# Kernel tuning notes

Measured on AMD Instinct MI355X. Metric: run time of the kernel, lower is better.

Reference implementation:

```python
import jax, jax.numpy as jnp
import numpy as np

NUM_GRAPHS = 64
NUM_LAYERS = 3
HEADS = 4
HID = 64
DMODEL = HEADS * HID  # 256
NUM_EDGE_TYPES = 8
NUM_CLASSES = 2
N_NODES = 30000
N_EDGES = 240000


def setup_inputs() -> dict:
    key = jax.random.key(0)
    ks = jax.random.split(key, 16)
    s = 0.05
    x = jax.random.normal(ks[0], (N_NODES, DMODEL), jnp.float32)
    edge_index = jax.random.randint(ks[1], (2, N_EDGES), 0, N_NODES)
    batch = jnp.sort(jax.random.randint(ks[2], (N_NODES,), 0, NUM_GRAPHS))
    edge_type_ids = jax.random.randint(ks[3], (N_EDGES,), 0, NUM_EDGE_TYPES)
    # stacked per-layer conv params (all layers are DMODEL -> HEADS*HID = DMODEL)
    Wq = jax.random.normal(ks[4], (NUM_LAYERS, DMODEL, DMODEL), jnp.float32) * s
    bq = jax.random.normal(ks[5], (NUM_LAYERS, DMODEL), jnp.float32) * s
    Wk = jax.random.normal(ks[6], (NUM_LAYERS, DMODEL, DMODEL), jnp.float32) * s
    bk = jax.random.normal(ks[7], (NUM_LAYERS, DMODEL), jnp.float32) * s
    Wv = jax.random.normal(ks[8], (NUM_LAYERS, DMODEL, DMODEL), jnp.float32) * s
    bv = jax.random.normal(ks[9], (NUM_LAYERS, DMODEL), jnp.float32) * s
    Eemb = jax.random.normal(ks[10], (NUM_LAYERS, NUM_EDGE_TYPES, DMODEL), jnp.float32) * s
    # 1-layer GRU (PyTorch layout: [3*hid, in], gate order r, z, n)
    W_ih = jax.random.normal(ks[11], (3 * HID, DMODEL), jnp.float32) * s
    b_ih = jax.random.normal(ks[12], (3 * HID,), jnp.float32) * s
    W_hh = jax.random.normal(ks[13], (3 * HID, HID), jnp.float32) * s
    b_hh = jax.random.normal(ks[14], (3 * HID,), jnp.float32) * s
    W_fc = jax.random.normal(ks[15], (NUM_CLASSES, HID), jnp.float32) * s
    b_fc = jnp.zeros((NUM_CLASSES,), jnp.float32)
    return dict(x=x, edge_index=edge_index, batch=batch, edge_type_ids=edge_type_ids,
                Wq=Wq, bq=bq, Wk=Wk, bk=bk, Wv=Wv, bv=bv, Eemb=Eemb,
                W_ih=W_ih, b_ih=b_ih, W_hh=W_hh, b_hh=b_hh, W_fc=W_fc, b_fc=b_fc)


def reference(x, edge_index, batch, edge_type_ids, Wq, bq, Wk, bk, Wv, bv, Eemb,
              W_ih, b_ih, W_hh, b_hh, W_fc, b_fc):
    N = x.shape[0]
    src, dst = edge_index[0], edge_index[1]  # messages flow src -> dst
    scale = 1.0 / jnp.sqrt(jnp.float32(HID))
    for l in range(NUM_LAYERS):
        q = (x @ Wq[l] + bq[l]).reshape(N, HEADS, HID)
        k_all = x @ Wk[l] + bk[l]  # [N, DMODEL]
        v_all = x @ Wv[l] + bv[l]
        ete = Eemb[l][edge_type_ids]  # edge-type conditioning, [E, DMODEL]
        k = (k_all[src] + ete).reshape(-1, HEADS, HID)
        v = (v_all[src] + ete).reshape(-1, HEADS, HID)
        scores = jnp.einsum('ehd,ehd->eh', q[dst], k) * scale  # [E, H]
        # per-destination-node segment softmax (stable)
        m = jax.ops.segment_max(scores, dst, num_segments=N)
        ex = jnp.exp(scores - m[dst])
        den = jax.ops.segment_sum(ex, dst, num_segments=N)
        alpha = ex / (den[dst] + 1e-16)
        agg = jax.ops.segment_sum(alpha[..., None] * v, dst, num_segments=N)
        x = jax.nn.elu(agg.reshape(N, DMODEL))
    # global mean pool over graphs
    cnt = jax.ops.segment_sum(jnp.ones((N,), x.dtype), batch, num_segments=NUM_GRAPHS)
    g = jax.ops.segment_sum(x, batch, num_segments=NUM_GRAPHS) / jnp.maximum(cnt, 1.0)[:, None]
    # single GRU step from h0 = 0 (seq_len == 1)
    h0 = jnp.zeros((NUM_GRAPHS, HID), x.dtype)
    gi = g @ W_ih.T + b_ih
    gh = h0 @ W_hh.T + b_hh
    ir, iz, inn = jnp.split(gi, 3, axis=-1)
    hr, hz, hn = jnp.split(gh, 3, axis=-1)
    r = jax.nn.sigmoid(ir + hr)
    z = jax.nn.sigmoid(iz + hz)
    n = jnp.tanh(inn + r * hn)
    h = (1.0 - z) * n + z * h0
    return h @ W_fc.T + b_fc  # [NUM_GRAPHS, NUM_CLASSES]
```

## Files before the change

### kernel.cpp

```cpp
#include <hip/hip_runtime.h>
#include <math.h>

#define N_NODES 30000
#define N_EDGES 240000
#define DMODEL 256
#define NETYPES 8
#define NGRAPHS 64
#define NLAYERS 3

typedef __attribute__((ext_vector_type(8))) short short8;
typedef __attribute__((ext_vector_type(4))) float f32x4;

__device__ __forceinline__ unsigned short f2bf(float f) {
  union { float f; unsigned u; } v; v.f = f;
  unsigned r = v.u + 0x7FFF + ((v.u >> 16) & 1);
  return (unsigned short)(r >> 16);
}
__device__ __forceinline__ float bf2f(unsigned short h) {
  union { unsigned u; float f; } v; v.u = ((unsigned)h) << 16;
  return v.f;
}

__device__ __forceinline__ void async_g2l(const unsigned short* g, unsigned short* l) {
  __builtin_amdgcn_global_load_lds(
      (const __attribute__((address_space(1))) void*)g,
      (__attribute__((address_space(3))) void*)l, 16, 0, 0);
}

__global__ void k_count_deg(const int* __restrict__ dst, int* __restrict__ deg) {
  int e = blockIdx.x * blockDim.x + threadIdx.x;
  if (e < N_EDGES) atomicAdd(&deg[dst[e]], 1);
}

__global__ __launch_bounds__(1024) void k_scan(const int* __restrict__ deg,
                                               int* __restrict__ rowstart,
                                               int* __restrict__ cursor) {
  const int C = 30;
  int tid = threadIdx.x;
  int base = tid * C;
  int vals[C];
  int sum = 0;
#pragma unroll
  for (int j = 0; j < C; ++j) {
    int idx = base + j;
    int v = (idx < N_NODES) ? deg[idx] : 0;
    vals[j] = sum;
    sum += v;
  }
  int lane = tid & 63, wv = tid >> 6;
  int s = sum;
#pragma unroll
  for (int off = 1; off < 64; off <<= 1) {
    int t2 = __shfl_up(s, off);
    if (lane >= off) s += t2;
  }
  __shared__ int wsum[16];
  if (lane == 63) wsum[wv] = s;
  __syncthreads();
  if (tid == 0) {
    int a = 0;
#pragma unroll
    for (int i = 0; i < 16; ++i) { int t2 = wsum[i]; wsum[i] = a; a += t2; }
    rowstart[N_NODES] = a;
  }
  __syncthreads();
  int texcl = wsum[wv] + (s - sum);
#pragma unroll
  for (int j = 0; j < C; ++j) {
    int idx = base + j;
    if (idx < N_NODES) {
      int p = texcl + vals[j];
      rowstart[idx] = p;
      cursor[idx]   = p;
    }
  }
}

__global__ void k_scatter(const int* __restrict__ src, const int* __restrict__ dst,
                          const int* __restrict__ etype, int* __restrict__ cursor,
                          int* __restrict__ packed) {
  int e = blockIdx.x * blockDim.x + threadIdx.x;
  if (e < N_EDGES) {
    int p = atomicAdd(&cursor[dst[e]], 1);
    packed[p] = src[e] * NETYPES + etype[e];
  }
}

__global__ __launch_bounds__(256) void k_cvt_w(
    const float* __restrict__ Wq, const float* __restrict__ Wk, const float* __restrict__ Wv,
    unsigned short* __restrict__ wthi) {
  __shared__ float tile[32][33];
  int k0 = blockIdx.x * 32;
  int n0g = blockIdx.y * 32;
  int l = blockIdx.z;
  int which = n0g >> 8;
  int col0 = n0g & 255;
  const float* W = (which == 0) ? Wq : ((which == 1) ? Wk : Wv);
  int c = threadIdx.x & 31, r = threadIdx.x >> 5;
#pragma unroll
  for (int rr = 0; rr < 4; ++rr) {
    int kk = r + rr * 8;
    tile[kk][c] = W[(size_t)l * 65536 + (size_t)(k0 + kk) * 256 + col0 + c];
  }
  __syncthreads();
  int kk = threadIdx.x & 31, nn0 = threadIdx.x >> 5;
#pragma unroll
  for (int rr = 0; rr < 4; ++rr) {
    int nn = nn0 + rr * 8;
    wthi[((size_t)l * 768 + n0g + nn) * 256 + k0 + kk] = f2bf(tile[kk][nn]);
  }
}

__global__ void k_cvt_b(const float* __restrict__ bq, const float* __restrict__ bk,
                        const float* __restrict__ bv, float* __restrict__ bcat) {
  int idx = blockIdx.x * 256 + threadIdx.x;
  if (idx >= NLAYERS * 768) return;
  int n = idx % 768, l = idx / 768;
  int which = n >> 8, col = n & 255;
  const float* b = (which == 0) ? bq : ((which == 1) ? bk : bv);
  bcat[idx] = b[l * 256 + col];
}

__global__ void k_cvt_x(const float* __restrict__ x, unsigned short* __restrict__ xhi,
                        unsigned short* __restrict__ xlo) {
  int i = blockIdx.x * 256 + threadIdx.x;
  if (i < N_NODES * 256) {
    float v = x[i];
    unsigned short h = f2bf(v);
    xhi[i] = h;
    xlo[i] = f2bf(v - bf2f(h));
  }
}

__global__ __launch_bounds__(256) void k_gemm_mfma(
    const unsigned short* __restrict__ Ahi, const unsigned short* __restrict__ Alo,
    const unsigned short* __restrict__ Bhi,
    const float* __restrict__ bcat, float* __restrict__ qbuf,
    unsigned short* __restrict__ kv) {
  __shared__ unsigned short smem[2 * 12288];

  int tid = threadIdx.x;
  int lane = tid & 63, wave = tid >> 6;
  int bx = blockIdx.x;
  int xcd = bx & 7, slot = bx >> 3;
  int rt = xcd + (slot / 6) * 8;
  if (rt >= 235) return;
  int row0 = rt * 128;
  int n0 = (slot % 6) * 128;
  int wm = (wave >> 1) * 64, wn = (wave & 1) * 64;
  int quad = lane >> 4, l16 = lane & 15;
  int chunk = lane & 3;
  int srow = wave * 32 + (lane >> 2);

  f32x4 acc[4][4];
#pragma unroll
  for (int i = 0; i < 4; ++i)
#pragma unroll
    for (int j = 0; j < 4; ++j) acc[i][j] = (f32x4)(0.f);

  auto STAGE = [&](int k0, int b) {
    unsigned short* s = smem + b * 12288;
#pragma unroll
    for (int j = 0; j < 2; ++j) {
      int r = srow + j * 16;
      int ldsoff = wave * 1024 + j * 512;
      int garA = row0 + r; if (garA >= N_NODES) garA = N_NODES - 1;
      size_t aoff = (size_t)garA * 256 + k0 + chunk * 8;
      async_g2l(Ahi + aoff, s + ldsoff);
      async_g2l(Alo + aoff, s + 4096 + ldsoff);
      size_t boff = (size_t)(n0 + r) * 256 + k0 + chunk * 8;
      async_g2l(Bhi + boff, s + 8192 + ldsoff);
    }
  };

  STAGE(0, 0);
#pragma unroll
  for (int k = 0; k < 8; ++k) {
    int cur = k & 1;
    if (k < 7) {
      STAGE((k + 1) * 32, cur ^ 1);
      asm volatile("s_waitcnt vmcnt(6)" ::: "memory");
    } else {
      asm volatile("s_waitcnt vmcnt(0)" ::: "memory");
    }
    __builtin_amdgcn_s_barrier();

    const unsigned short* sAhi = smem + cur * 12288;
    const unsigned short* sAlo = sAhi + 4096;
    const unsigned short* sBhi = sAhi + 8192;
    short8 ah[4], al[4], bh[4];
#pragma unroll
    for (int i = 0; i < 4; ++i) {
      int off = (wm + i * 16 + l16) * 32 + quad * 8;
      ah[i] = *(const short8*)(sAhi + off);
      al[i] = *(const short8*)(sAlo + off);
    }
#pragma unroll
    for (int j = 0; j < 4; ++j) {
      int off = (wn + j * 16 + l16) * 32 + quad * 8;
      bh[j] = *(const short8*)(sBhi + off);
    }
#pragma unroll
    for (int i = 0; i < 4; ++i)
#pragma unroll
      for (int j = 0; j < 4; ++j) {
        acc[i][j] = __builtin_amdgcn_mfma_f32_16x16x32_bf16(ah[i], bh[j], acc[i][j], 0, 0, 0);
        acc[i][j] = __builtin_amdgcn_mfma_f32_16x16x32_bf16(al[i], bh[j], acc[i][j], 0, 0, 0);
      }
    __builtin_amdgcn_s_barrier();
  }

  float bj[4];
#pragma unroll
  for (int j = 0; j < 4; ++j) bj[j] = bcat[n0 + wn + j * 16 + l16];
  bool isq = (n0 < 256);
#pragma unroll
  for (int i = 0; i < 4; ++i) {
    int rowb = row0 + wm + i * 16 + quad * 4;
#pragma unroll
    for (int r = 0; r < 4; ++r) {
      int grow = rowb + r;
      if (grow < N_NODES) {
        if (isq) {
          float* cp = qbuf + (size_t)grow * 256 + n0 + wn + l16;
#pragma unroll
          for (int j = 0; j < 4; ++j) cp[j * 16] = acc[i][j][r] + bj[j];
        } else {
          unsigned short* cp = kv + (size_t)grow * 512 + (n0 - 256) + wn + l16;
#pragma unroll
          for (int j = 0; j < 4; ++j) cp[j * 16] = f2bf(acc[i][j][r] + bj[j]);
        }
      }
    }
  }
}

__global__ __launch_bounds__(256) void k_attn(
    const float* __restrict__ qbuf, const unsigned short* __restrict__ kv,
    const int* __restrict__ rowstart, const int* __restrict__ packed,
    const float* __restrict__ Eemb_l,
    unsigned short* __restrict__ xhi, unsigned short* __restrict__ xlo) {
  __shared__ float ete_s[NETYPES * 256];
  int t = threadIdx.x;
#pragma unroll
  for (int i = 0; i < NETYPES; ++i) ete_s[i * 256 + t] = Eemb_l[i * 256 + t];
  __syncthreads();
  int lane = t & 63;
  int n = blockIdx.x * 4 + (t >> 6);
  float4 q4 = ((const float4*)(qbuf + (size_t)n * 256))[lane];
  int rs = rowstart[n], re = rowstart[n + 1];
  float l1 = 0.f, ax1 = 0.f, ay1 = 0.f, az1 = 0.f, aw1 = 0.f;
  float l2 = 0.f, ax2 = 0.f, ay2 = 0.f, az2 = 0.f, aw2 = 0.f;
  int i = rs;
  for (; i + 2 <= re; i += 2) {
    int pkA = packed[i], pkB = packed[i + 1];
    const unsigned short* baseA = kv + (size_t)(pkA >> 3) * 512;
    const unsigned short* baseB = kv + (size_t)(pkB >> 3) * 512;
    ushort4 kA = ((const ushort4*)baseA)[lane];
    ushort4 vA = ((const ushort4*)(baseA + 256))[lane];
    ushort4 kB = ((const ushort4*)baseB)[lane];
    ushort4 vB = ((const ushort4*)(baseB + 256))[lane];
    float4 eA = ((const float4*)(ete_s + (pkA & 7) * 256))[lane];
    float4 eB = ((const float4*)(ete_s + (pkB & 7) * 256))[lane];
    float pA = (bf2f(kA.x) + eA.x) * q4.x + (bf2f(kA.y) + eA.y) * q4.y +
               (bf2f(kA.z) + eA.z) * q4.z + (bf2f(kA.w) + eA.w) * q4.w;
    float pB = (bf2f(kB.x) + eB.x) * q4.x + (bf2f(kB.y) + eB.y) * q4.y +
               (bf2f(kB.z) + eB.z) * q4.z + (bf2f(kB.w) + eB.w) * q4.w;
    pA += __shfl_xor(pA, 1); pB += __shfl_xor(pB, 1);
    pA += __shfl_xor(pA, 2); pB += __shfl_xor(pB, 2);
    pA += __shfl_xor(pA, 4); pB += __shfl_xor(pB, 4);
    pA += __shfl_xor(pA, 8); pB += __shfl_xor(pB, 8);
    float e1 = __expf(pA * 0.125f);
    float e2 = __expf(pB * 0.125f);
    l1 += e1; l2 += e2;
    ax1 = fmaf(e1, bf2f(vA.x) + eA.x, ax1);
    ay1 = fmaf(e1, bf2f(vA.y) + eA.y, ay1);
    az1 = fmaf(e1, bf2f(vA.z) + eA.z, az1);
    aw1 = fmaf(e1, bf2f(vA.w) + eA.w, aw1);
    ax2 = fmaf(e2, bf2f(vB.x) + eB.x, ax2);
    ay2 = fmaf(e2, bf2f(vB.y) + eB.y, ay2);
    az2 = fmaf(e2, bf2f(vB.z) + eB.z, az2);
    aw2 = fmaf(e2, bf2f(vB.w) + eB.w, aw2);
  }
  if (i < re) {
    int pk = packed[i];
    const unsigned short* base = kv + (size_t)(pk >> 3) * 512;
    ushort4 kh = ((const ushort4*)base)[lane];
    ushort4 vh = ((const ushort4*)(base + 256))[lane];
    float4 e4 = ((const float4*)(ete_s + (pk & 7) * 256))[lane];
    float p = (bf2f(kh.x) + e4.x) * q4.x + (bf2f(kh.y) + e4.y) * q4.y +
              (bf2f(kh.z) + e4.z) * q4.z + (bf2f(kh.w) + e4.w) * q4.w;
    p += __shfl_xor(p, 1);
    p += __shfl_xor(p, 2);
    p += __shfl_xor(p, 4);
    p += __shfl_xor(p, 8);
    float e1 = __expf(p * 0.125f);
    l1 += e1;
    ax1 = fmaf(e1, bf2f(vh.x) + e4.x, ax1);
    ay1 = fmaf(e1, bf2f(vh.y) + e4.y, ay1);
    az1 = fmaf(e1, bf2f(vh.z) + e4.z, az1);
    aw1 = fmaf(e1, bf2f(vh.w) + e4.w, aw1);
  }
  float l = l1 + l2;
  float inv = 1.f / (l + 1e-16f);
  float4 o;
  o.x = (ax1 + ax2) * inv; o.y = (ay1 + ay2) * inv;
  o.z = (az1 + az2) * inv; o.w = (aw1 + aw2) * inv;
  o.x = o.x > 0.f ? o.x : expm1f(o.x);
  o.y = o.y > 0.f ? o.y : expm1f(o.y);
  o.z = o.z > 0.f ? o.z : expm1f(o.z);
  o.w = o.w > 0.f ? o.w : expm1f(o.w);
  unsigned short h0 = f2bf(o.x), h1 = f2bf(o.y), h2 = f2bf(o.z), h3 = f2bf(o.w);
  ushort4 hv, lv;
  hv.x = h0; hv.y = h1; hv.z = h2; hv.w = h3;
  lv.x = f2bf(o.x - bf2f(h0)); lv.y = f2bf(o.y - bf2f(h1));
  lv.z = f2bf(o.z - bf2f(h2)); lv.w = f2bf(o.w - bf2f(h3));
  size_t base_o = (size_t)n * 256 + lane * 4;
  *(ushort4*)(xhi + base_o) = hv;
  *(ushort4*)(xlo + base_o) = lv;
}

__global__ __launch_bounds__(256) void k_pool_partial(
    const unsigned short* __restrict__ xhi, const unsigned short* __restrict__ xlo,
    const int* __restrict__ batch, float* __restrict__ gacc) {
  int t = threadIdx.x;
  int base = blockIdx.x * 128;
  int end = base + 128; if (end > N_NODES) end = N_NODES;
  __shared__ int bsh[128];
  if (t < 128 && base + t < N_NODES) bsh[t] = batch[base + t];
  __syncthreads();
  float acc = 0.f;
  int cur = bsh[0];
  for (int n = base; n < end; ++n) {
    int g = bsh[n - base];
    if (g != cur) {
      atomicAdd(&gacc[cur * 256 + t], acc);
      acc = 0.f; cur = g;
    }
    size_t idx = (size_t)n * 256 + t;
    acc += bf2f(xhi[idx]) + bf2f(xlo[idx]);
  }
  atomicAdd(&gacc[cur * 256 + t], acc);
}

__device__ inline int lower_bound_dev(const int* a, int n, int val) {
  int lo = 0, hi = n;
  while (lo < hi) {
    int mid = (lo + hi) >> 1;
    if (a[mid] < val) lo = mid + 1; else hi = mid;
  }
  return lo;
}

__global__ __launch_bounds__(256) void k_gru_fc(
    const float* __restrict__ gacc, const int* __restrict__ batch,
    const float* __restrict__ W_ih, const float* __restrict__ b_ih,
    const float* __restrict__ b_hh, const float* __restrict__ W_fc,
    const float* __restrict__ b_fc, float* __restrict__ out) {
  __shared__ float gv[256];
  __shared__ float gates[192];
  __shared__ float h[64];
  int gr = blockIdx.x, t = threadIdx.x;
  int s0 = lower_bound_dev(batch, N_NODES, gr);
  int e0 = lower_bound_dev(batch, N_NODES, gr + 1);
  float c = (e0 > s0) ? (float)(e0 - s0) : 1.f;
  gv[t] = gacc[gr * 256 + t] / c;
  __syncthreads();
  if (t < 192) {
    const float* wr = W_ih + t * 256;
    float s = b_ih[t];
    for (int k = 0; k < 256; ++k) s = fmaf(gv[k], wr[k], s);
    gates[t] = s;
  }
  __syncthreads();
  if (t < 64) {
    float r  = 1.f / (1.f + expf(-(gates[t] + b_hh[t])));
    float z  = 1.f / (1.f + expf(-(gates[64 + t] + b_hh[64 + t])));
    float nn = tanhf(gates[128 + t] + r * b_hh[128 + t]);
    h[t] = (1.f - z) * nn;
  }
  __syncthreads();
  if (t < 2) {
    const float* wr = W_fc + t * 64;
    float s = b_fc[t];
    for (int k = 0; k < 64; ++k) s = fmaf(h[k], wr[k], s);
    out[gr * 2 + t] = s;
  }
}

extern "C" void kernel_launch(void* const* d_in, const int* in_sizes, int n_in,
                              void* d_out, int out_size, void* d_ws, size_t ws_size,
                              hipStream_t stream) {
  const float* x     = (const float*)d_in[0];
  const int* edge_index = (const int*)d_in[1];
  const int* batch   = (const int*)d_in[2];
  const int* etype   = (const int*)d_in[3];
  const float* Wq    = (const float*)d_in[4];
  const float* bq    = (const float*)d_in[5];
  const float* Wk    = (const float*)d_in[6];
  const float* bk    = (const float*)d_in[7];
  const float* Wv    = (const float*)d_in[8];
  const float* bv    = (const float*)d_in[9];
  const float* Eemb  = (const float*)d_in[10];
  const float* W_ih  = (const float*)d_in[11];
  const float* b_ih  = (const float*)d_in[12];
  const float* b_hh  = (const float*)d_in[14];
  const float* W_fc  = (const float*)d_in[15];
  const float* b_fc  = (const float*)d_in[16];
  float* out = (float*)d_out;

  const int* src = edge_index;
  const int* dst = edge_index + N_EDGES;

  float* qbuf  = (float*)d_ws;
  float* gacc  = qbuf + (size_t)N_NODES * 256;
  float* bcat  = gacc + NGRAPHS * 256;
  unsigned short* kv   = (unsigned short*)(bcat + NLAYERS * 768);
  unsigned short* xhi  = kv + (size_t)N_NODES * 512;
  unsigned short* xlo  = xhi + (size_t)N_NODES * 256;
  unsigned short* wthi = xlo + (size_t)N_NODES * 256;
  int* deg      = (int*)(wthi + (size_t)NLAYERS * 768 * 256);
  int* rowstart = deg + N_NODES;
  int* cursor   = rowstart + N_NODES + 1;
  int* packed   = cursor + N_NODES;

  hipMemsetAsync(deg, 0, N_NODES * sizeof(int), stream);
  hipMemsetAsync(gacc, 0, NGRAPHS * 256 * sizeof(float), stream);
  k_count_deg<<<(N_EDGES + 255) / 256, 256, 0, stream>>>(dst, deg);
  k_scan<<<1, 1024, 0, stream>>>(deg, rowstart, cursor);
  k_scatter<<<(N_EDGES + 255) / 256, 256, 0, stream>>>(src, dst, etype, cursor, packed);

  k_cvt_w<<<dim3(8, 24, 3), 256, 0, stream>>>(Wq, Wk, Wv, wthi);
  k_cvt_b<<<(NLAYERS * 768 + 255) / 256, 256, 0, stream>>>(bq, bk, bv, bcat);
  k_cvt_x<<<(N_NODES * 256 + 255) / 256, 256, 0, stream>>>(x, xhi, xlo);

  for (int l = 0; l < NLAYERS; ++l) {
    k_gemm_mfma<<<1440, 256, 0, stream>>>(
        xhi, xlo, wthi + (size_t)l * 768 * 256,
        bcat + l * 768, qbuf, kv);
    k_attn<<<N_NODES / 4, 256, 0, stream>>>(qbuf, kv, rowstart, packed,
                                            Eemb + (size_t)l * NETYPES * 256, xhi, xlo);
  }
  k_pool_partial<<<(N_NODES + 127) / 128, 256, 0, stream>>>(xhi, xlo, batch, gacc);
  k_gru_fc<<<NGRAPHS, 256, 0, stream>>>(gacc, batch, W_ih, b_ih, b_hh, W_fc, b_fc, out);
}
```

Before: 461.8 us.

## Software-pipeline edge gathers in attention kernel with wave-wide index prefetch

The attention kernel now loads up to 64 edge indices per destination node in one coalesced wave load and broadcasts them with shuffles. It then double-buffers K/V/edge-embedding gathers in groups of four edges, issuing the next group's loads before computing the current one. This is meant to hide gather latency by keeping more memory requests in flight. In exchange it uses more registers, which may lower occupancy, and nodes with more than 64 edges fall back to a serial tail loop.

```diff
diff --git a/kernel.cpp b/kernel.cpp
--- a/kernel.cpp
+++ b/kernel.cpp
@@ -235,6 +235,36 @@
   }
 }
 
+#define LOAD1(pk, K, V, E)                                       \
+  { const unsigned short* b_ = kv + (size_t)((pk) >> 3) * 512;   \
+    K = ((const ushort4*)b_)[lane];                              \
+    V = ((const ushort4*)(b_ + 256))[lane];                      \
+    E = ((const float4*)(ete_s + ((pk) & 7) * 256))[lane]; }
+
+#define EDGE1(K, V, E)                                                 \
+  { float p_ = (bf2f(K.x) + E.x) * q4.x + (bf2f(K.y) + E.y) * q4.y +   \
+               (bf2f(K.z) + E.z) * q4.z + (bf2f(K.w) + E.w) * q4.w;    \
+    p_ += __shfl_xor(p_, 1); p_ += __shfl_xor(p_, 2);                  \
+    p_ += __shfl_xor(p_, 4); p_ += __shfl_xor(p_, 8);                  \
+    float e_ = __expf(p_ * 0.125f);                                    \
+    lsum += e_;                                                        \
+    ax = fmaf(e_, bf2f(V.x) + E.x, ax);                                \
+    ay = fmaf(e_, bf2f(V.y) + E.y, ay);                                \
+    az = fmaf(e_, bf2f(V.z) + E.z, az);                                \
+    aw = fmaf(e_, bf2f(V.w) + E.w, aw); }
+
+#define LOAD4(s, c)                                                    \
+  { int p0_ = __shfl(mypk, (c));     int p1_ = __shfl(mypk, (c) + 1);  \
+    int p2_ = __shfl(mypk, (c) + 2); int p3_ = __shfl(mypk, (c) + 3);  \
+    LOAD1(p0_, k##s##0, v##s##0, e##s##0)                              \
+    LOAD1(p1_, k##s##1, v##s##1, e##s##1)                              \
+    LOAD1(p2_, k##s##2, v##s##2, e##s##2)                              \
+    LOAD1(p3_, k##s##3, v##s##3, e##s##3) }
+
+#define COMP4(s)                                                        \
+    EDGE1(k##s##0, v##s##0, e##s##0) EDGE1(k##s##1, v##s##1, e##s##1)   \
+    EDGE1(k##s##2, v##s##2, e##s##2) EDGE1(k##s##3, v##s##3, e##s##3)
+
 __global__ __launch_bounds__(256) void k_attn(
     const float* __restrict__ qbuf, const unsigned short* __restrict__ kv,
     const int* __restrict__ rowstart, const int* __restrict__ packed,
@@ -249,63 +279,48 @@
   int n = blockIdx.x * 4 + (t >> 6);
   float4 q4 = ((const float4*)(qbuf + (size_t)n * 256))[lane];
   int rs = rowstart[n], re = rowstart[n + 1];
-  float l1 = 0.f, ax1 = 0.f, ay1 = 0.f, az1 = 0.f, aw1 = 0.f;
-  float l2 = 0.f, ax2 = 0.f, ay2 = 0.f, az2 = 0.f, aw2 = 0.f;
-  int i = rs;
-  for (; i + 2 <= re; i += 2) {
-    int pkA = packed[i], pkB = packed[i + 1];
-    const unsigned short* baseA = kv + (size_t)(pkA >> 3) * 512;
-    const unsigned short* baseB = kv + (size_t)(pkB >> 3) * 512;
-    ushort4 kA = ((const ushort4*)baseA)[lane];
-    ushort4 vA = ((const ushort4*)(baseA + 256))[lane];
-    ushort4 kB = ((const ushort4*)baseB)[lane];
-    ushort4 vB = ((const ushort4*)(baseB + 256))[lane];
-    float4 eA = ((const float4*)(ete_s + (pkA & 7) * 256))[lane];
-    float4 eB = ((const float4*)(ete_s + (pkB & 7) * 256))[lane];
-    float pA = (bf2f(kA.x) + eA.x) * q4.x + (bf2f(kA.y) + eA.y) * q4.y +
-               (bf2f(kA.z) + eA.z) * q4.z + (bf2f(kA.w) + eA.w) * q4.w;
-    float pB = (bf2f(kB.x) + eB.x) * q4.x + (bf2f(kB.y) + eB.y) * q4.y +
-               (bf2f(kB.z) + eB.z) * q4.z + (bf2f(kB.w) + eB.w) * q4.w;
-    pA += __shfl_xor(pA, 1); pB += __shfl_xor(pB, 1);
-    pA += __shfl_xor(pA, 2); pB += __shfl_xor(pB, 2);
-    pA += __shfl_xor(pA, 4); pB += __shfl_xor(pB, 4);
-    pA += __shfl_xor(pA, 8); pB += __shfl_xor(pB, 8);
-    float e1 = __expf(pA * 0.125f);
-    float e2 = __expf(pB * 0.125f);
-    l1 += e1; l2 += e2;
-    ax1 = fmaf(e1, bf2f(vA.x) + eA.x, ax1);
-    ay1 = fmaf(e1, bf2f(vA.y) + eA.y, ay1);
-    az1 = fmaf(e1, bf2f(vA.z) + eA.z, az1);
-    aw1 = fmaf(e1, bf2f(vA.w) + eA.w, aw1);
-    ax2 = fmaf(e2, bf2f(vB.x) + eB.x, ax2);
-    ay2 = fmaf(e2, bf2f(vB.y) + eB.y, ay2);
-    az2 = fmaf(e2, bf2f(vB.z) + eB.z, az2);
-    aw2 = fmaf(e2, bf2f(vB.w) + eB.w, aw2);
-  }
-  if (i < re) {
-    int pk = packed[i];
-    const unsigned short* base = kv + (size_t)(pk >> 3) * 512;
-    ushort4 kh = ((const ushort4*)base)[lane];
-    ushort4 vh = ((const ushort4*)(base + 256))[lane];
-    float4 e4 = ((const float4*)(ete_s + (pk & 7) * 256))[lane];
-    float p = (bf2f(kh.x) + e4.x) * q4.x + (bf2f(kh.y) + e4.y) * q4.y +
-              (bf2f(kh.z) + e4.z) * q4.z + (bf2f(kh.w) + e4.w) * q4.w;
-    p += __shfl_xor(p, 1);
-    p += __shfl_xor(p, 2);
-    p += __shfl_xor(p, 4);
-    p += __shfl_xor(p, 8);
-    float e1 = __expf(p * 0.125f);
-    l1 += e1;
-    ax1 = fmaf(e1, bf2f(vh.x) + e4.x, ax1);
-    ay1 = fmaf(e1, bf2f(vh.y) + e4.y, ay1);
-    az1 = fmaf(e1, bf2f(vh.z) + e4.z, az1);
-    aw1 = fmaf(e1, bf2f(vh.w) + e4.w, aw1);
-  }
-  float l = l1 + l2;
-  float inv = 1.f / (l + 1e-16f);
+  int deg = re - rs;
+
+  float lsum = 0.f, ax = 0.f, ay = 0.f, az = 0.f, aw = 0.f;
+
+  int mypk = 0;
+  if (deg > 0) mypk = packed[rs + (lane < deg ? lane : deg - 1)];
+
+  int nfast = deg <= 64 ? deg : 64;
+  int nc = nfast >> 2;
+
+  ushort4 kA0, kA1, kA2, kA3, vA0, vA1, vA2, vA3;
+  ushort4 kB0, kB1, kB2, kB3, vB0, vB1, vB2, vB3;
+  float4 eA0, eA1, eA2, eA3, eB0, eB1, eB2, eB3;
+
+  if (nc >= 1) LOAD4(A, 0)
+  if (nc >= 2) LOAD4(B, 4)
+  for (int cc = 0; cc < nc; ++cc) {
+    if ((cc & 1) == 0) {
+      COMP4(A)
+      if (cc + 2 < nc) LOAD4(A, (cc + 2) * 4)
+    } else {
+      COMP4(B)
+      if (cc + 2 < nc) LOAD4(B, (cc + 2) * 4)
+    }
+  }
+  for (int i = nc * 4; i < nfast; ++i) {
+    int pk_ = __shfl(mypk, i);
+    ushort4 kh, vh; float4 e4;
+    LOAD1(pk_, kh, vh, e4)
+    EDGE1(kh, vh, e4)
+  }
+  for (int i = rs + 64; i < re; ++i) {
+    int pk_ = packed[i];
+    ushort4 kh, vh; float4 e4;
+    LOAD1(pk_, kh, vh, e4)
+    EDGE1(kh, vh, e4)
+  }
+
+  float inv = 1.f / (lsum + 1e-16f);
   float4 o;
-  o.x = (ax1 + ax2) * inv; o.y = (ay1 + ay2) * inv;
-  o.z = (az1 + az2) * inv; o.w = (aw1 + aw2) * inv;
+  o.x = ax * inv; o.y = ay * inv;
+  o.z = az * inv; o.w = aw * inv;
   o.x = o.x > 0.f ? o.x : expm1f(o.x);
   o.y = o.y > 0.f ? o.y : expm1f(o.y);
   o.z = o.z > 0.f ? o.z : expm1f(o.z);
```

New measurement: 501.0 us. +8.5%, slower.
